# Optimization experiments

Measured on AMD Instinct MI355X. Metric: run time of the kernel, lower is better.

## Reference

```python
import jax, jax.numpy as jnp
import numpy as np
import math

N, E, C, H = 16384, 8192, 256, 8
NNZ = 262144  # incidence pairs, avg vertex degree 16


def setup_inputs() -> dict:
    key = jax.random.key(0)
    ks = jax.random.split(key, 12)
    s = 1.0 / math.sqrt(C)
    inp = {
        "X": jax.random.normal(ks[0], (N, C), dtype=jnp.float32),
        "v_ids": jax.random.randint(ks[1], (NNZ,), 0, N, dtype=jnp.int32),
        "e_ids": jax.random.randint(ks[2], (NNZ,), 0, E, dtype=jnp.int32),
        # Linear params stored as [in, out]; y = x @ W + b  (matches torch x @ W.T + b)
        "Wq": jax.random.uniform(ks[3], (C, C), jnp.float32, -s, s),
        "bq": jax.random.uniform(ks[4], (C,), jnp.float32, -s, s),
        "Wk": jax.random.uniform(ks[5], (C, C), jnp.float32, -s, s),
        "bk": jax.random.uniform(ks[6], (C,), jnp.float32, -s, s),
        "Wv": jax.random.uniform(ks[7], (C, C), jnp.float32, -s, s),
        "bv": jax.random.uniform(ks[8], (C,), jnp.float32, -s, s),
        "Wke": jax.random.uniform(ks[9], (C, C), jnp.float32, -s, s),
        "bke": jax.random.uniform(ks[10], (C,), jnp.float32, -s, s),
    }
    return inp


def reference(X, v_ids, e_ids, Wq, bq, Wk, bk, Wv, bv, Wke, bke):
    d = C // H
    scale = 1.0 / math.sqrt(d)

    Q = (X @ Wq + bq).reshape(N, H, d)
    K = (X @ Wk + bk).reshape(N, H, d)
    V = (X @ Wv + bv).reshape(N, H, d)

    # hg.v2e_aggregation(X, 'mean'): segment-mean of incident vertex features per hyperedge
    sums = jax.ops.segment_sum(X[v_ids], e_ids, num_segments=E)          # [E, C]
    cnt = jax.ops.segment_sum(jnp.ones((NNZ,), X.dtype), e_ids, num_segments=E)
    Xe = sums / jnp.maximum(cnt, 1.0)[:, None]                            # [E, C]

    Ke = Xe @ Wke + bke                                                   # [E, C]
    Qe = X @ Wq + bq                                                      # [N, C]

    # per-node attention over heads: [N, H, H]
    attn_n = jax.nn.softmax(jnp.einsum('nhd,ngd->nhg', Q, K) * scale, axis=-1)
    X_node = jnp.einsum('nhg,ngd->nhd', attn_n, V).reshape(N, C)          # [N, C]

    # node -> hyperedge attention: [N, E]
    attn_e = jax.nn.softmax((Qe @ Ke.T) * scale, axis=-1)
    X_hyperedge = attn_e @ Xe                                             # [N, C]

    out = X_node + X_hyperedge
    # is_last=False: ReLU; bn=None; dropout in eval mode (identity)
    return jax.nn.relu(out)
```

## Files before the change

### kernel.cpp

```cpp
#include <hip/hip_runtime.h>

typedef unsigned short u16;
typedef unsigned int u32;
typedef __attribute__((ext_vector_type(4))) float f32x4;
typedef __attribute__((ext_vector_type(16))) float f32x16;
typedef __attribute__((ext_vector_type(8))) short bf16x8;
typedef __attribute__((ext_vector_type(4))) short bf16x4;
typedef __attribute__((ext_vector_type(4))) u16 u16x4;
typedef __attribute__((ext_vector_type(2))) u32 u32x2;
typedef __attribute__((ext_vector_type(4))) u32 u32x4;

#define N_NODES 16384
#define N_EDGES 8192
#define FK_SCALE 0.17677669529663687f
#define LOG2E 1.4426950408889634f
#define C1EXP (FK_SCALE * LOG2E)

typedef const u32 __attribute__((address_space(1))) gu32;
typedef u32 __attribute__((address_space(3))) lu32;

__device__ __forceinline__ void gl_lds16(const void* g, void* l) {
  __builtin_amdgcn_global_load_lds((gu32*)g, (lu32*)l, 16, 0, 0);
}

__device__ __forceinline__ float b2f(u16 u) {
  return __builtin_bit_cast(float, (u32)u << 16);
}
__device__ __forceinline__ u16 f2b(float f) {
  u32 u = __builtin_bit_cast(u32, f);
  u += 0x7fffu + ((u >> 16) & 1u);
  return (u16)(u >> 16);
}

__device__ __forceinline__ u32 cvtpk(float a, float b) {
  u32 r;
  asm("v_cvt_pk_bf16_f32 %0, %1, %2" : "=v"(r) : "v"(a), "v"(b));
  return r;
}

__device__ __forceinline__ u32x2 swap32v(u32 x, u32 y) {
#if __has_builtin(__builtin_amdgcn_permlane32_swap)
  auto r = __builtin_amdgcn_permlane32_swap(x, y, false, false);
  u32x2 out = {(u32)r[0], (u32)r[1]};
  return out;
#else
  u32 px = __shfl_xor(x, 32, 64), py = __shfl_xor(y, 32, 64);
  bool hi = (threadIdx.x & 32) != 0;
  u32x2 out = {hi ? x : py, hi ? px : y};
  return out;
#endif
}

__global__ __launch_bounds__(256) void k_prep(const float* __restrict__ X,
                                              const int* __restrict__ e_ids,
                                              u16* __restrict__ Xb,
                                              int* __restrict__ hist,
                                              const float* __restrict__ Wq,
                                              const float* __restrict__ Wk,
                                              const float* __restrict__ Wv,
                                              const float* __restrict__ Wke,
                                              const float* __restrict__ bq,
                                              const float* __restrict__ bk,
                                              const float* __restrict__ bv,
                                              const float* __restrict__ bke,
                                              u16* __restrict__ Wt,
                                              float* __restrict__ bcat) {
  __shared__ float tile[64][65];
  int b = blockIdx.x;
  int tid = threadIdx.x;
  if (b < 4096) {
    int i = b * 256 + tid;
    f32x4 v = *(const f32x4*)(X + (size_t)i * 4);
    u16x4 r;
    r.x = f2b(v.x); r.y = f2b(v.y); r.z = f2b(v.z); r.w = f2b(v.w);
    *(u16x4*)(Xb + (size_t)i * 4) = r;
    if (tid < 64) atomicAdd(&hist[e_ids[b * 64 + tid]], 1);
    return;
  }
  int local = b - 4096;
  int w = local >> 4, rem = local & 15;
  int k0 = (rem >> 2) * 64, n0 = (rem & 3) * 64;
  const float* W = (w == 0) ? Wq : (w == 1) ? Wk : (w == 2) ? Wv : Wke;
  if (rem == 0) {
    const float* bb = (w == 0) ? bq : (w == 1) ? bk : (w == 2) ? bv : bke;
    bcat[w * 256 + tid] = bb[tid];
  }
#pragma unroll
  for (int i = 0; i < 16; i++) {
    int idx = i * 256 + tid;
    int kr = idx >> 6, nc = idx & 63;
    tile[nc][kr] = W[(k0 + kr) * 256 + n0 + nc];
  }
  __syncthreads();
#pragma unroll
  for (int i = 0; i < 16; i++) {
    int idx = i * 256 + tid;
    int nr = idx >> 6, kc = idx & 63;
    Wt[w * 65536 + (n0 + nr) * 256 + k0 + kc] = f2b(tile[nr][kc]);
  }
}

__global__ __launch_bounds__(256) void k_scan(const int* __restrict__ hist,
                                              int* __restrict__ eoff,
                                              int* __restrict__ cur) {
  __shared__ int ts[256];
  int t = threadIdx.x;
  int base = t * 32;
  int vals[32];
  int s = 0;
#pragma unroll
  for (int i = 0; i < 32; i++) { vals[i] = hist[base + i]; s += vals[i]; }
  ts[t] = s;
  __syncthreads();
  for (int off = 1; off < 256; off <<= 1) {
    int v = (t >= off) ? ts[t - off] : 0;
    __syncthreads();
    ts[t] += v;
    __syncthreads();
  }
  int ex = ts[t] - s;
#pragma unroll
  for (int i = 0; i < 32; i++) {
    eoff[base + i] = ex;
    cur[base + i] = ex;
    ex += vals[i];
  }
  if (t == 255) eoff[8192] = ex;
}

__global__ __launch_bounds__(256) void k_perm(const int* __restrict__ v_ids,
                                              const int* __restrict__ e_ids,
                                              int* __restrict__ cur,
                                              int* __restrict__ perm) {
  int base = blockIdx.x * 1024 + threadIdx.x;
#pragma unroll
  for (int k = 0; k < 4; k++) {
    int i = base + k * 256;
    int e = e_ids[i];
    int v = v_ids[i];
    int pos = atomicAdd(&cur[e], 1);
    perm[pos] = v;
  }
}

__global__ __launch_bounds__(256) void k_gg(const u16* __restrict__ Xb,
                                            const int* __restrict__ perm,
                                            const int* __restrict__ eoff,
                                            u16* __restrict__ Xe,
                                            u16* __restrict__ XeTc,
                                            const u16* __restrict__ Wt,
                                            const float* __restrict__ bcat,
                                            u16* __restrict__ QKV) {
  __shared__ u16 As[128 * 64];
  __shared__ u16 Bs[128 * 64];
  int b = blockIdx.x;
  int tid = threadIdx.x;
  int wave = tid >> 6, lane = tid & 63;
  if (b < 768) {
    int quad = lane >> 4, l16 = lane & 15;
    int wm = wave >> 1, wn = wave & 1;
    int mtile = (b & 127) * 128, ntile = (b >> 7) * 128;
    const u16* Ap = Xb + (size_t)mtile * 256;
    const u16* Bp = Wt + (size_t)ntile * 256;
    f32x4 acc[4][4];
#pragma unroll
    for (int am = 0; am < 4; am++)
#pragma unroll
      for (int bn = 0; bn < 4; bn++) acc[am][bn] = (f32x4){0.f, 0.f, 0.f, 0.f};
    for (int ks = 0; ks < 4; ks++) {
      __syncthreads();
#pragma unroll
      for (int i = 0; i < 4; i++) {
        int s = i * 256 + tid;
        int r = s >> 3, c = s & 7;
        gl_lds16(Ap + r * 256 + ks * 64 + ((c ^ (r & 7)) << 3), As + s * 8);
      }
#pragma unroll
      for (int i = 0; i < 4; i++) {
        int s = i * 256 + tid;
        int r = s >> 3, c = s & 7;
        gl_lds16(Bp + r * 256 + ks * 64 + ((c ^ (r & 7)) << 3), Bs + s * 8);
      }
      __syncthreads();
#pragma unroll
      for (int kc = 0; kc < 2; kc++) {
        bf16x8 a[4], bb[4];
        int cc = kc * 4 + quad;
#pragma unroll
        for (int am = 0; am < 4; am++) {
          int rl = wm * 64 + am * 16 + l16;
          a[am] = *(const bf16x8*)(As + rl * 64 + ((cc ^ (rl & 7)) << 3));
        }
#pragma unroll
        for (int bn = 0; bn < 4; bn++) {
          int rl = wn * 64 + bn * 16 + l16;
          bb[bn] = *(const bf16x8*)(Bs + rl * 64 + ((cc ^ (rl & 7)) << 3));
        }
#pragma unroll
        for (int am = 0; am < 4; am++)
#pragma unroll
          for (int bn = 0; bn < 4; bn++)
            acc[am][bn] = __builtin_amdgcn_mfma_f32_16x16x32_bf16(a[am], bb[bn], acc[am][bn], 0, 0, 0);
      }
    }
#pragma unroll
    for (int am = 0; am < 4; am++)
#pragma unroll
      for (int bn = 0; bn < 4; bn++)
#pragma unroll
        for (int r = 0; r < 4; r++) {
          int row = mtile + wm * 64 + am * 16 + quad * 4 + r;
          int col = ntile + wn * 64 + bn * 16 + l16;
          QKV[(size_t)row * 768 + col] = f2b(acc[am][bn][r] + bcat[col]);
        }
    return;
  }
  int e = (b - 768) * 4 + wave;
  int start = eoff[e], end = eoff[e + 1];
  int cnt = end - start;
  int pidx = 0;
  if (lane < cnt) pidx = perm[start + lane];
  f32x4 acc = {0.f, 0.f, 0.f, 0.f};
  int n1 = cnt < 64 ? cnt : 64;
  for (int j = 0; j < n1; j++) {
    int v = __shfl(pidx, j, 64);
    bf16x4 x = *(const bf16x4*)(Xb + (size_t)v * 256 + lane * 4);
#pragma unroll
    for (int c = 0; c < 4; c++) acc[c] += b2f((u16)x[c]);
  }
  for (int j = start + 64; j < end; j++) {
    int v = perm[j];
    bf16x4 x = *(const bf16x4*)(Xb + (size_t)v * 256 + lane * 4);
#pragma unroll
    for (int c = 0; c < 4; c++) acc[c] += b2f((u16)x[c]);
  }
  float inv = 1.0f / fmaxf((float)cnt, 1.0f);
  u16x4 r;
  r.x = f2b(acc.x * inv); r.y = f2b(acc.y * inv);
  r.z = f2b(acc.z * inv); r.w = f2b(acc.w * inv);
  *(u16x4*)(Xe + (size_t)e * 256 + lane * 4) = r;
  size_t tb = (size_t)(e >> 3) * 2048 + (e & 7);
  XeTc[tb + (lane * 4 + 0) * 8] = r.x;
  XeTc[tb + (lane * 4 + 1) * 8] = r.y;
  XeTc[tb + (lane * 4 + 2) * 8] = r.z;
  XeTc[tb + (lane * 4 + 3) * 8] = r.w;
}

__global__ __launch_bounds__(256) void k_gemmke(const u16* __restrict__ A,
                                                const u16* __restrict__ Wt,
                                                const float* __restrict__ bias,
                                                u16* __restrict__ KebT) {
  __shared__ u16 As[128 * 64];
  __shared__ u16 Bs[128 * 64];
  int tid = threadIdx.x;
  int wave = tid >> 6, lane = tid & 63;
  int quad = lane >> 4, l16 = lane & 15;
  int wm = wave >> 1, wn = wave & 1;
  int mtile = blockIdx.x * 128, ntile = blockIdx.y * 128;
  const u16* Ap = A + (size_t)mtile * 256;
  const u16* Bp = Wt + (size_t)ntile * 256;
  f32x4 acc[4][4];
#pragma unroll
  for (int am = 0; am < 4; am++)
#pragma unroll
    for (int bn = 0; bn < 4; bn++) acc[am][bn] = (f32x4){0.f, 0.f, 0.f, 0.f};
  for (int ks = 0; ks < 4; ks++) {
    __syncthreads();
#pragma unroll
    for (int i = 0; i < 4; i++) {
      int s = i * 256 + tid;
      int r = s >> 3, c = s & 7;
      gl_lds16(Ap + r * 256 + ks * 64 + ((c ^ (r & 7)) << 3), As + s * 8);
    }
#pragma unroll
    for (int i = 0; i < 4; i++) {
      int s = i * 256 + tid;
      int r = s >> 3, c = s & 7;
      gl_lds16(Bp + r * 256 + ks * 64 + ((c ^ (r & 7)) << 3), Bs + s * 8);
    }
    __syncthreads();
#pragma unroll
    for (int kc = 0; kc < 2; kc++) {
      bf16x8 a[4], b[4];
      int cc = kc * 4 + quad;
#pragma unroll
      for (int am = 0; am < 4; am++) {
        int rl = wm * 64 + am * 16 + l16;
        a[am] = *(const bf16x8*)(As + rl * 64 + ((cc ^ (rl & 7)) << 3));
      }
#pragma unroll
      for (int bn = 0; bn < 4; bn++) {
        int rl = wn * 64 + bn * 16 + l16;
        b[bn] = *(const bf16x8*)(Bs + rl * 64 + ((cc ^ (rl & 7)) << 3));
      }
#pragma unroll
      for (int am = 0; am < 4; am++)
#pragma unroll
        for (int bn = 0; bn < 4; bn++)
          acc[am][bn] = __builtin_amdgcn_mfma_f32_16x16x32_bf16(a[am], b[bn], acc[am][bn], 0, 0, 0);
    }
  }
#pragma unroll
  for (int am = 0; am < 4; am++)
#pragma unroll
    for (int bn = 0; bn < 4; bn++)
#pragma unroll
      for (int r = 0; r < 4; r++) {
        int row = mtile + wm * 64 + am * 16 + quad * 4 + r;
        int col = ntile + wn * 64 + bn * 16 + l16;
        KebT[(size_t)(col >> 3) * 65536 + row * 8 + (col & 7)] = f2b(acc[am][bn][r] + bias[col]);
      }
}

__device__ __forceinline__ void stage_k(const u16* __restrict__ KebT, u16* KeL,
                                        int kbase, int tid) {
#pragma unroll
  for (int i = 0; i < 4; i++) {
    int s = i * 256 + tid;
    int c = s >> 5, r = s & 31;
    gl_lds16(KebT + ((size_t)c * 8192 + kbase + r) * 8, KeL + s * 8);
  }
}
__device__ __forceinline__ void stage_v(const u16* __restrict__ XeTc, u16* VLT,
                                        int ktg, int tid) {
  int kb8 = ktg * 4;
#pragma unroll
  for (int i = 0; i < 4; i++) {
    int s = i * 256 + tid;
    int kc = s >> 8, ch = s & 255;
    gl_lds16(XeTc + ((size_t)(kb8 + kc) * 256 + ch) * 8, VLT + s * 8);
  }
}

__global__ __launch_bounds__(256, 2) void k_flash(const u16* __restrict__ QKV,
                                                  const u16* __restrict__ KebT,
                                                  const u16* __restrict__ XeTc,
                                                  u16* __restrict__ Op,
                                                  float* __restrict__ Lv) {
  extern __shared__ u16 sm[];
  u16* KeL = sm;
  u16* VLT = sm + 8192;
  int tid = threadIdx.x;
  int wave = tid >> 6, lane = tid & 63;
  int l31 = lane & 31, half = lane >> 5;
  int qt = blockIdx.x & 127;
  int split = blockIdx.x >> 7;
  int rowq = qt * 128 + wave * 32 + l31;

  bf16x8 qf[16];
#pragma unroll
  for (int ks = 0; ks < 16; ks++)
    qf[ks] = *(const bf16x8*)(QKV + (size_t)rowq * 768 + ks * 16 + half * 8);

  f32x16 o[8];
#pragma unroll
  for (int i = 0; i < 8; i++)
#pragma unroll
    for (int r = 0; r < 16; r++) o[i][r] = 0.f;
  float lsum = 0.f;

  stage_k(KebT, KeL, split * 2048, tid);

  const u16* kp = KeL + half * 256 + l31 * 8;
  const u16* vp = VLT + half * 2048 + l31 * 8;

  for (int ktl = 0; ktl < 64; ktl++) {
    int ktg = split * 64 + ktl;
    __syncthreads();
    stage_v(XeTc, VLT, ktg, tid);

    f32x16 s0;
#pragma unroll
    for (int r = 0; r < 16; r++) s0[r] = 0.f;
    __builtin_amdgcn_s_setprio(1);
#pragma unroll
    for (int ks = 0; ks < 16; ks++) {
      bf16x8 ka = *(const bf16x8*)(kp + ks * 512);
      s0 = __builtin_amdgcn_mfma_f32_32x32x16_bf16(ka, qf[ks], s0, 0, 0, 0);
    }
    __builtin_amdgcn_s_setprio(0);

    u32 w[8];
#pragma unroll
    for (int i = 0; i < 8; i++) {
      float e0 = __builtin_amdgcn_exp2f(s0[2 * i] * C1EXP);
      float e1 = __builtin_amdgcn_exp2f(s0[2 * i + 1] * C1EXP);
      lsum += e0 + e1;
      w[i] = cvtpk(e0, e1);
    }
    {
      u32x2 r;
      r = swap32v(w[2], w[0]); w[2] = r.x; w[0] = r.y;
      r = swap32v(w[3], w[1]); w[3] = r.x; w[1] = r.y;
      r = swap32v(w[6], w[4]); w[6] = r.x; w[4] = r.y;
      r = swap32v(w[7], w[5]); w[7] = r.x; w[5] = r.y;
    }
    u32x4 p0v = {w[0], w[1], w[2], w[3]};
    u32x4 p1v = {w[4], w[5], w[6], w[7]};
    bf16x8 pf0 = __builtin_bit_cast(bf16x8, p0v);
    bf16x8 pf1 = __builtin_bit_cast(bf16x8, p1v);

    __syncthreads();
    if (ktl + 1 < 64) stage_k(KebT, KeL, (ktg + 1) * 32, tid);

    __builtin_amdgcn_s_setprio(1);
#pragma unroll
    for (int ct = 0; ct < 8; ct++) {
      const u16* vpc = vp + ct * 256;
      o[ct] = __builtin_amdgcn_mfma_f32_32x32x16_bf16(pf0, *(const bf16x8*)(vpc), o[ct], 0, 0, 0);
      o[ct] = __builtin_amdgcn_mfma_f32_32x32x16_bf16(pf1, *(const bf16x8*)(vpc + 4096), o[ct], 0, 0, 0);
    }
    __builtin_amdgcn_s_setprio(0);
  }

  lsum += __shfl_xor(lsum, 32, 64);
  if (lane < 32) Lv[split * N_NODES + qt * 128 + wave * 32 + l31] = lsum;

  size_t obase = (size_t)split * N_NODES * 256;
#pragma unroll
  for (int ct = 0; ct < 8; ct++)
#pragma unroll
    for (int reg = 0; reg < 16; reg++) {
      int row = qt * 128 + wave * 32 + (reg & 3) + 8 * (reg >> 2) + 4 * half;
      int col = ct * 32 + l31;
      Op[obase + (size_t)row * 256 + col] = f2b(o[ct][reg]);
    }
}

__global__ __launch_bounds__(256) void k_comb(const u16* __restrict__ QKV,
                                              const u16* __restrict__ Op,
                                              const float* __restrict__ Lv,
                                              float* __restrict__ out) {
  int idx = blockIdx.x * 256 + threadIdx.x;
  int n = idx >> 6, lane = idx & 63;
  int h = lane >> 3, g = lane & 7;
  const u16* base = QKV + n * 768;
  const bf16x8* qp = (const bf16x8*)(base + h * 32);
  const bf16x8* kp = (const bf16x8*)(base + 256 + g * 32);
  float s = 0.f;
#pragma unroll
  for (int t = 0; t < 4; t++) {
    bf16x8 qv = qp[t], kv = kp[t];
#pragma unroll
    for (int j = 0; j < 8; j++) s += b2f((u16)qv[j]) * b2f((u16)kv[j]);
  }
  s *= FK_SCALE;
  float mx = s;
#pragma unroll
  for (int off = 1; off < 8; off <<= 1) mx = fmaxf(mx, __shfl_xor(mx, off, 64));
  float p = __builtin_amdgcn_exp2f((s - mx) * LOG2E);
  float lsum = p;
#pragma unroll
  for (int off = 1; off < 8; off <<= 1) lsum += __shfl_xor(lsum, off, 64);
  float attn = p / lsum;
  float a4[4] = {0.f, 0.f, 0.f, 0.f};
#pragma unroll
  for (int g2 = 0; g2 < 8; g2++) {
    float a = __shfl(attn, (lane & 56) | g2, 64);
    bf16x4 vv = *(const bf16x4*)(base + 512 + g2 * 32 + g * 4);
#pragma unroll
    for (int j = 0; j < 4; j++) a4[j] += a * b2f((u16)vv[j]);
  }
  int c4 = lane * 4;
  float L = 0.f;
#pragma unroll
  for (int sl = 0; sl < 4; sl++) L += Lv[sl * N_NODES + n];
  f32x4 acc = {0.f, 0.f, 0.f, 0.f};
#pragma unroll
  for (int sp = 0; sp < 4; sp++) {
    u16x4 ov = *(const u16x4*)(Op + (size_t)sp * N_NODES * 256 + (size_t)n * 256 + c4);
    acc.x += b2f(ov.x);
    acc.y += b2f(ov.y);
    acc.z += b2f(ov.z);
    acc.w += b2f(ov.w);
  }
  float invL = 1.0f / L;
  f32x4 res;
  res.x = fmaxf(acc.x * invL + a4[0], 0.f);
  res.y = fmaxf(acc.y * invL + a4[1], 0.f);
  res.z = fmaxf(acc.z * invL + a4[2], 0.f);
  res.w = fmaxf(acc.w * invL + a4[3], 0.f);
  *(f32x4*)(out + (size_t)n * 256 + c4) = res;
}

extern "C" void kernel_launch(void* const* d_in, const int* in_sizes, int n_in,
                              void* d_out, int out_size, void* d_ws, size_t ws_size,
                              hipStream_t stream) {
  const float* X = (const float*)d_in[0];
  const int* v_ids = (const int*)d_in[1];
  const int* e_ids = (const int*)d_in[2];
  const float* Wq = (const float*)d_in[3];
  const float* bq = (const float*)d_in[4];
  const float* Wk = (const float*)d_in[5];
  const float* bk = (const float*)d_in[6];
  const float* Wv = (const float*)d_in[7];
  const float* bv = (const float*)d_in[8];
  const float* Wke = (const float*)d_in[9];
  const float* bke = (const float*)d_in[10];
  float* out = (float*)d_out;

  char* ws = (char*)d_ws;
  u16* Xb = (u16*)(ws);
  u16* QKV = (u16*)(ws + 8388608);
  u16* Wt = (u16*)(ws + 33554432);
  float* bcat = (float*)(ws + 34078720);
  int* hist = (int*)(ws + 34082816);
  int* eoff = (int*)(ws + 34115584);
  int* cur = (int*)(ws + 34152448);
  int* perm = (int*)(ws + 34185216);
  u16* Xe = (u16*)(ws + 35233792);
  u16* XeTc = (u16*)(ws + 39428096);
  u16* KebT = (u16*)(ws + 43622400);
  u16* Op = (u16*)(ws + 64593920);
  float* Lv = (float*)(ws + 98148352);

  hipMemsetAsync(hist, 0, 32768, stream);
  k_prep<<<4160, 256, 0, stream>>>(X, e_ids, Xb, hist, Wq, Wk, Wv, Wke,
                                   bq, bk, bv, bke, Wt, bcat);
  k_scan<<<1, 256, 0, stream>>>(hist, eoff, cur);
  k_perm<<<256, 256, 0, stream>>>(v_ids, e_ids, cur, perm);
  k_gg<<<2816, 256, 0, stream>>>(Xb, perm, eoff, Xe, XeTc, Wt, bcat, QKV);
  k_gemmke<<<dim3(64, 2), 256, 0, stream>>>(Xe, Wt + 3 * 65536, bcat + 768, KebT);
  hipFuncSetAttribute((const void*)k_flash, hipFuncAttributeMaxDynamicSharedMemorySize,
                      32768);
  k_flash<<<512, 256, 32768, stream>>>(QKV, KebT, XeTc, Op, Lv);
  k_comb<<<4096, 256, 0, stream>>>(QKV, Op, Lv, out);
}
```

Measured before the change: 319.7 us.

## Double-buffer K and V tiles in LDS for flash attention kernel

Replaces the single-buffered K/V staging, which needed two barriers per tile, with a ping-pong scheme over two 32 KB LDS buffers. Each step issues async loads for the next tile into the other buffer and then computes on the current one, using one barrier per step. The aim is to hide global-to-LDS latency behind MFMA work and remove a barrier. In exchange, LDS per block doubles to 64 KB, which may limit how many blocks fit per CU.

After: 325.0 us. Within noise of the previous version (+1.6%).

```diff
diff --git a/kernel.cpp b/kernel.cpp
--- a/kernel.cpp
+++ b/kernel.cpp
@@ -338,8 +338,6 @@
                                                   u16* __restrict__ Op,
                                                   float* __restrict__ Lv) {
   extern __shared__ u16 sm[];
-  u16* KeL = sm;
-  u16* VLT = sm + 8192;
   int tid = threadIdx.x;
   int wave = tid >> 6, lane = tid & 63;
   int l31 = lane & 31, half = lane >> 5;
@@ -359,59 +357,59 @@
     for (int r = 0; r < 16; r++) o[i][r] = 0.f;
   float lsum = 0.f;
 
-  stage_k(KebT, KeL, split * 2048, tid);
-
-  const u16* kp = KeL + half * 256 + l31 * 8;
-  const u16* vp = VLT + half * 2048 + l31 * 8;
-
-  for (int ktl = 0; ktl < 64; ktl++) {
-    int ktg = split * 64 + ktl;
-    __syncthreads();
-    stage_v(XeTc, VLT, ktg, tid);
-
-    f32x16 s0;
-#pragma unroll
-    for (int r = 0; r < 16; r++) s0[r] = 0.f;
-    __builtin_amdgcn_s_setprio(1);
-#pragma unroll
-    for (int ks = 0; ks < 16; ks++) {
-      bf16x8 ka = *(const bf16x8*)(kp + ks * 512);
-      s0 = __builtin_amdgcn_mfma_f32_32x32x16_bf16(ka, qf[ks], s0, 0, 0, 0);
-    }
-    __builtin_amdgcn_s_setprio(0);
-
-    u32 w[8];
-#pragma unroll
-    for (int i = 0; i < 8; i++) {
-      float e0 = __builtin_amdgcn_exp2f(s0[2 * i] * C1EXP);
-      float e1 = __builtin_amdgcn_exp2f(s0[2 * i + 1] * C1EXP);
-      lsum += e0 + e1;
-      w[i] = cvtpk(e0, e1);
-    }
-    {
-      u32x2 r;
-      r = swap32v(w[2], w[0]); w[2] = r.x; w[0] = r.y;
-      r = swap32v(w[3], w[1]); w[3] = r.x; w[1] = r.y;
-      r = swap32v(w[6], w[4]); w[6] = r.x; w[4] = r.y;
-      r = swap32v(w[7], w[5]); w[7] = r.x; w[5] = r.y;
-    }
-    u32x4 p0v = {w[0], w[1], w[2], w[3]};
-    u32x4 p1v = {w[4], w[5], w[6], w[7]};
-    bf16x8 pf0 = __builtin_bit_cast(bf16x8, p0v);
-    bf16x8 pf1 = __builtin_bit_cast(bf16x8, p1v);
-
-    __syncthreads();
-    if (ktl + 1 < 64) stage_k(KebT, KeL, (ktg + 1) * 32, tid);
-
-    __builtin_amdgcn_s_setprio(1);
-#pragma unroll
-    for (int ct = 0; ct < 8; ct++) {
-      const u16* vpc = vp + ct * 256;
-      o[ct] = __builtin_amdgcn_mfma_f32_32x32x16_bf16(pf0, *(const bf16x8*)(vpc), o[ct], 0, 0, 0);
-      o[ct] = __builtin_amdgcn_mfma_f32_32x32x16_bf16(pf1, *(const bf16x8*)(vpc + 4096), o[ct], 0, 0, 0);
-    }
-    __builtin_amdgcn_s_setprio(0);
-  }
+  stage_k(KebT, sm, split * 2048, tid);
+  stage_v(XeTc, sm + 8192, split * 64, tid);
+
+#define FLASH_STEP(RB, T)                                                          \
+  {                                                                                \
+    __syncthreads();            \
+    int ktg = split * 64 + (T);                                                    \
+    if ((T) + 1 < 64) {                                                            \
+      stage_k(KebT, sm + ((RB) ^ 1) * 16384, (ktg + 1) * 32, tid);                 \
+      stage_v(XeTc, sm + ((RB) ^ 1) * 16384 + 8192, ktg + 1, tid);                 \
+    }                                                                              \
+    const u16* kp = sm + (RB) * 16384 + half * 256 + l31 * 8;                      \
+    const u16* vp = sm + (RB) * 16384 + 8192 + half * 2048 + l31 * 8;              \
+    f32x16 s0;                                                                     \
+    _Pragma("unroll") for (int r = 0; r < 16; r++) s0[r] = 0.f;                    \
+    __builtin_amdgcn_s_setprio(1);                                                 \
+    _Pragma("unroll") for (int ks = 0; ks < 16; ks++) {                            \
+      bf16x8 ka = *(const bf16x8*)(kp + ks * 512);                                 \
+      s0 = __builtin_amdgcn_mfma_f32_32x32x16_bf16(ka, qf[ks], s0, 0, 0, 0);       \
+    }                                                                              \
+    __builtin_amdgcn_s_setprio(0);                                                 \
+    u32 w[8];                                                                      \
+    _Pragma("unroll") for (int i = 0; i < 8; i++) {                                \
+      float e0 = __builtin_amdgcn_exp2f(s0[2 * i] * C1EXP);                        \
+      float e1 = __builtin_amdgcn_exp2f(s0[2 * i + 1] * C1EXP);                    \
+      lsum += e0 + e1;                                                             \
+      w[i] = cvtpk(e0, e1);                                                        \
+    }                                                                              \
+    {                                                                              \
+      u32x2 r;                                                                     \
+      r = swap32v(w[2], w[0]); w[2] = r.x; w[0] = r.y;                             \
+      r = swap32v(w[3], w[1]); w[3] = r.x; w[1] = r.y;                             \
+      r = swap32v(w[6], w[4]); w[6] = r.x; w[4] = r.y;                             \
+      r = swap32v(w[7], w[5]); w[7] = r.x; w[5] = r.y;                             \
+    }                                                                              \
+    u32x4 p0v = {w[0], w[1], w[2], w[3]};                                          \
+    u32x4 p1v = {w[4], w[5], w[6], w[7]};                                          \
+    bf16x8 pf0 = __builtin_bit_cast(bf16x8, p0v);                                  \
+    bf16x8 pf1 = __builtin_bit_cast(bf16x8, p1v);                                  \
+    __builtin_amdgcn_s_setprio(1);                                                 \
+    _Pragma("unroll") for (int ct = 0; ct < 8; ct++) {                             \
+      const u16* vpc = vp + ct * 256;                                              \
+      o[ct] = __builtin_amdgcn_mfma_f32_32x32x16_bf16(pf0, *(const bf16x8*)(vpc), o[ct], 0, 0, 0); \
+      o[ct] = __builtin_amdgcn_mfma_f32_32x32x16_bf16(pf1, *(const bf16x8*)(vpc + 4096), o[ct], 0, 0, 0); \
+    }                                                                              \
+    __builtin_amdgcn_s_setprio(0);                                                 \
+  }
+
+  for (int t2 = 0; t2 < 64; t2 += 2) {
+    FLASH_STEP(0, t2);
+    FLASH_STEP(1, t2 + 1);
+  }
+#undef FLASH_STEP
 
   lsum += __shfl_xor(lsum, 32, 64);
   if (lane < 32) Lv[split * N_NODES + qt * 128 + wave * 32 + l31] = lsum;
@@ -522,7 +520,7 @@
   k_gg<<<2816, 256, 0, stream>>>(Xb, perm, eoff, Xe, XeTc, Wt, bcat, QKV);
   k_gemmke<<<dim3(64, 2), 256, 0, stream>>>(Xe, Wt + 3 * 65536, bcat + 768, KebT);
   hipFuncSetAttribute((const void*)k_flash, hipFuncAttributeMaxDynamicSharedMemorySize,
-                      32768);
-  k_flash<<<512, 256, 32768, stream>>>(QKV, KebT, XeTc, Op, Lv);
+                      65536);
+  k_flash<<<512, 256, 65536, stream>>>(QKV, KebT, XeTc, Op, Lv);
   k_comb<<<4096, 256, 0, stream>>>(QKV, Op, Lv, out);
 }
```
